# Kernel tuning notes

Measured on AMD Instinct MI355X. Metric: run time of the kernel, lower is better.

## Reference

```python
import jax, jax.numpy as jnp
import numpy as np
from jax import lax

N_KERNELS = 11
N_GRAMS = 3
EMB = 300
CONV_OUT = 128
B, QLEN, DLEN = 128, 30, 256


def _kernel_mus(n):
    mus = [1.0]
    bin_size = 2.0 / (n - 1)
    mus.append(1 - bin_size / 2)
    for i in range(1, n - 1):
        mus.append(mus[i] - bin_size)
    return mus


def _kernel_sigmas(n):
    bin_size = 2.0 / (n - 1)
    return [0.001] + [0.5 * bin_size] * (n - 1)


MU = jnp.asarray(np.array(_kernel_mus(N_KERNELS), dtype=np.float32))      # [K]
SIGMA = jnp.asarray(np.array(_kernel_sigmas(N_KERNELS), dtype=np.float32))  # [K]


def setup_inputs() -> dict:
    key = jax.random.key(0)
    ks = jax.random.split(key, 10)
    inp = {
        "query_embeddings": jax.random.normal(ks[0], (B, QLEN, EMB), jnp.float32),
        "document_embeddings": jax.random.normal(ks[1], (B, DLEN, EMB), jnp.float32),
        "query_pad_oov_mask": jnp.ones((B, QLEN), jnp.float32),
        "document_pad_oov_mask": jnp.ones((B, DLEN), jnp.float32),
    }
    # conv weights for n-gram sizes 1..3: [out_ch, in_ch, ksize]
    for i in range(1, N_GRAMS + 1):
        inp[f"conv_w{i}"] = jax.random.normal(ks[1 + i], (CONV_OUT, EMB, i), jnp.float32) * 0.05
        inp[f"conv_b{i}"] = jnp.zeros((CONV_OUT,), jnp.float32)
    inp["dense_w"] = jax.random.uniform(ks[9], (1, N_KERNELS * N_GRAMS * N_GRAMS), jnp.float32,
                                        minval=-0.014, maxval=0.014)
    return inp


def _conv_ngram(x, w, b):
    # x: [B, L, E]; w: [C, E, k]; right-pad by k-1 so output length == L (ConstantPad1d((0,k-1)))
    k = w.shape[-1]
    y = lax.conv_general_dilated(x.transpose(0, 2, 1), w, (1,), [(0, k - 1)],
                                 dimension_numbers=("NCH", "OIH", "NCH"))
    return jax.nn.relu(y + b[None, :, None]).transpose(0, 2, 1)  # [B, L, C]


def _kernel_pool(q, d, qd_mask, q_mask):
    # cosine matrix (AllenNLP CosineMatrixAttention: normalize with +1e-13 eps)
    qn = q / (jnp.linalg.norm(q, axis=-1, keepdims=True) + 1e-13)
    dn = d / (jnp.linalg.norm(d, axis=-1, keepdims=True) + 1e-13)
    cos = jnp.einsum("bqe,bde->bqd", qn, dn) * qd_mask  # [B, Q, D]
    # RBF soft-histogram kernels: [B, Q, D, K]
    k = jnp.exp(-(cos[..., None] - MU) ** 2 / (2.0 * SIGMA ** 2)) * qd_mask[..., None]
    per_kernel_query = k.sum(axis=2)  # [B, Q, K]
    log_pk = jnp.log(jnp.clip(per_kernel_query, 1e-10, None)) * 0.01
    return (log_pk * q_mask[..., None]).sum(axis=1)  # [B, K]


def reference(query_embeddings, document_embeddings, query_pad_oov_mask, document_pad_oov_mask,
              conv_w1, conv_b1, conv_w2, conv_b2, conv_w3, conv_b3, dense_w):
    qd_mask = query_pad_oov_mask[:, :, None] * document_pad_oov_mask[:, None, :]  # [B, Q, D]
    conv_params = [(conv_w1, conv_b1), (conv_w2, conv_b2), (conv_w3, conv_b3)]
    q_res = [_conv_ngram(query_embeddings, w, b) for w, b in conv_params]
    d_res = [_conv_ngram(document_embeddings, w, b) for w, b in conv_params]
    matched = [_kernel_pool(q_res[i], d_res[t], qd_mask, query_pad_oov_mask)
               for i in range(N_GRAMS) for t in range(N_GRAMS)]
    all_grams = jnp.concatenate(matched, axis=1)  # [B, K*9]
    return jnp.squeeze(all_grams @ dense_w.T, axis=1)  # [B]
```

## Files before the change

### kernel.cpp

```cpp
#include <hip/hip_runtime.h>
#include <math.h>


typedef __bf16 bf16x8 __attribute__((ext_vector_type(8)));
typedef float f32x4 __attribute__((ext_vector_type(4)));

#if __has_builtin(__builtin_amdgcn_exp2f)
#define EXP2F(x) __builtin_amdgcn_exp2f(x)
#else
#define EXP2F(x) exp2f(x)
#endif

#define AS_STRIDE 344

static __device__ __forceinline__ unsigned short f2bf(float f) {
  union { float f; unsigned int u; } v; v.f = f;
  unsigned int r = v.u + 0x7FFFu + ((v.u >> 16) & 1u);
  return (unsigned short)(r >> 16);
}

__global__ __launch_bounds__(256) void prep_w(
    const float* __restrict__ w1, const float* __restrict__ w2,
    const float* __restrict__ w3, unsigned short* __restrict__ wt2) {
  int idx = blockIdx.x * 256 + threadIdx.x;
  if (idx >= 245760) return;
  int jj   = idx & 7;
  int lane = (idx >> 3) & 63;
  int ec   = (idx >> 9) % 10;
  int cb   = (idx / 5120) & 7;
  int p    = idx / 40960;
  const float* w; int k, jt;
  if (p == 0)      { w = w1; k = 1; jt = 0; }
  else if (p <= 2) { w = w2; k = 2; jt = p - 1; }
  else             { w = w3; k = 3; jt = p - 3; }
  int c = cb * 16 + (lane & 15);
  int e = ec * 32 + (lane >> 4) * 8 + jj;
  float v = (e < 300) ? w[(c * 300 + e) * k + jt] : 0.0f;
  wt2[idx] = f2bf(v);
}

template<int NI>
__device__ __forceinline__ void conv_body(
    unsigned short* As, float* psq,
    const float* __restrict__ xs, int L, int l0, int b,
    const unsigned short* __restrict__ wt2,
    const float* __restrict__ b1, const float* __restrict__ b2,
    const float* __restrict__ b3,
    unsigned short* __restrict__ out) {
  constexpr int ROWS = NI * 16 + 2;
  constexpr int NR = NI * 16;
  const int t = threadIdx.x;
  const int w = __builtin_amdgcn_readfirstlane(t >> 6);
  const int lane = t & 63;
  const int quad = lane >> 4, lrow = lane & 15;

  for (int idx = t; idx < ROWS * 40; idx += 512) {
    int r = idx / 40, c = idx % 40;
    int l = l0 + r;
    int e = c * 8;
    float4 a = make_float4(0.f, 0.f, 0.f, 0.f);
    float4 cc = make_float4(0.f, 0.f, 0.f, 0.f);
    if (l < L) {
      const float* src = xs + (size_t)l * 300;
      if (e < 300)     a  = *reinterpret_cast<const float4*>(src + e);
      if (e + 4 < 300) cc = *reinterpret_cast<const float4*>(src + e + 4);
    }
    uint4 o;
    o.x = (unsigned int)f2bf(a.x) | ((unsigned int)f2bf(a.y) << 16);
    o.y = (unsigned int)f2bf(a.z) | ((unsigned int)f2bf(a.w) << 16);
    o.z = (unsigned int)f2bf(cc.x) | ((unsigned int)f2bf(cc.y) << 16);
    o.w = (unsigned int)f2bf(cc.z) | ((unsigned int)f2bf(cc.w) << 16);
    *reinterpret_cast<uint4*>(&As[r * AS_STRIDE + c * 8]) = o;
  }

  f32x4 acc[NI][3];
  #pragma unroll
  for (int ni = 0; ni < NI; ++ni)
    #pragma unroll
    for (int g = 0; g < 3; ++g) acc[ni][g] = (f32x4){0.f, 0.f, 0.f, 0.f};

  const unsigned short* wl = wt2 + (size_t)lane * 8;

  auto wfld = [&](bf16x8* dst, int ec) {
    #pragma unroll
    for (int p = 0; p < 6; ++p)
      dst[p] = *reinterpret_cast<const bf16x8*>(
          wl + ((((p * 8 + w) * 10 + ec) << 9)));
  };

  auto compute = [&](const bf16x8* wf, int ec) {
    bf16x8 xf[3][NI];
    #pragma unroll
    for (int j = 0; j < 3; ++j)
      #pragma unroll
      for (int ni = 0; ni < NI; ++ni)
        xf[j][ni] = *reinterpret_cast<const bf16x8*>(
            &As[(ni * 16 + lrow + j) * AS_STRIDE + ec * 32 + quad * 8]);
    const int PJ[6] = {0, 0, 1, 0, 1, 2};
    const int PG[6] = {0, 1, 1, 2, 2, 2};
    #pragma unroll
    for (int p = 0; p < 6; ++p)
      #pragma unroll
      for (int ni = 0; ni < NI; ++ni)
        acc[ni][PG[p]] = __builtin_amdgcn_mfma_f32_16x16x32_bf16(
            wf[p], xf[PJ[p]][ni], acc[ni][PG[p]], 0, 0, 0);
  };

  bf16x8 wfA[6], wfB[6];
  wfld(wfA, 0);
  __syncthreads();

  #pragma unroll
  for (int ec = 0; ec < 10; ec += 2) {
    wfld(wfB, ec + 1);
    compute(wfA, ec);
    if (ec + 2 < 10) wfld(wfA, ec + 2);
    compute(wfB, ec + 1);
  }

  const float* biases[3] = {b1, b2, b3};
  float4 bv[3];
  #pragma unroll
  for (int g = 0; g < 3; ++g)
    bv[g] = *reinterpret_cast<const float4*>(biases[g] + w * 16 + quad * 4);

  #pragma unroll
  for (int ni = 0; ni < NI; ++ni) {
    #pragma unroll
    for (int g = 0; g < 3; ++g) {
      float p = 0.f;
      #pragma unroll
      for (int r = 0; r < 4; ++r) {
        float y = fmaxf(acc[ni][g][r] + bv[g][r], 0.f);
        p += y * y;
      }
      p += __shfl_xor(p, 16);
      p += __shfl_xor(p, 32);
      if (lane < 16) psq[(w * 3 + g) * NR + ni * 16 + lrow] = p;
    }
  }
  __syncthreads();

  #pragma unroll
  for (int ni = 0; ni < NI; ++ni) {
    int row = ni * 16 + lrow;
    int l = l0 + row;
    if (l < L) {
      #pragma unroll
      for (int g = 0; g < 3; ++g) {
        float ssq = 0.f;
        #pragma unroll
        for (int wv = 0; wv < 8; ++wv) ssq += psq[(wv * 3 + g) * NR + row];
        float inv = 1.0f / (sqrtf(ssq) + 1e-13f);
        unsigned int pk[2];
        #pragma unroll
        for (int h = 0; h < 2; ++h) {
          float y0 = fmaxf(acc[ni][g][2 * h + 0] + bv[g][2 * h + 0], 0.f) * inv;
          float y1 = fmaxf(acc[ni][g][2 * h + 1] + bv[g][2 * h + 1], 0.f) * inv;
          pk[h] = (unsigned int)f2bf(y0) | ((unsigned int)f2bf(y1) << 16);
        }
        unsigned short* op = out + ((size_t)(g * 128 + b) * L + l) * 128 +
                             w * 16 + quad * 4;
        *reinterpret_cast<uint2*>(op) = make_uint2(pk[0], pk[1]);
      }
    }
  }
}

__global__ __launch_bounds__(512, 4) void conv_all(
    const float* __restrict__ qemb, const float* __restrict__ demb,
    const unsigned short* __restrict__ wt2,
    const float* __restrict__ b1, const float* __restrict__ b2,
    const float* __restrict__ b3,
    unsigned short* __restrict__ qn, unsigned short* __restrict__ dn) {
  __shared__ unsigned short As[34 * AS_STRIDE];
  __shared__ float psq[8 * 3 * 32];
  const int bi = blockIdx.x;
  if (bi < 1024)
    conv_body<2>(As, psq, demb + (size_t)(bi >> 3) * 256 * 300, 256,
                 (bi & 7) * 32, bi >> 3, wt2, b1, b2, b3, dn);
  else
    conv_body<2>(As, psq, qemb + (size_t)(bi - 1024) * 30 * 300, 30,
                 0, bi - 1024, wt2, b1, b2, b3, qn);
}

__global__ __launch_bounds__(512, 1) void pool_final(
    const unsigned short* __restrict__ qn, const unsigned short* __restrict__ dn,
    const float* __restrict__ qmask, const float* __restrict__ dmask,
    const float* __restrict__ dw, float* __restrict__ out) {
  const float A2[11] = {2.0f, 1.8f, 1.4f, 1.0f, 0.6f, 0.2f,
                        -0.2f, -0.6f, -1.0f, -1.4f, -1.8f};
  const float CC[11] = {-721347.52f, -58.429149f, -35.346028f, -18.033688f,
                        -6.4921277f, -0.72134752f, -0.72134752f, -6.4921277f,
                        -18.033688f, -35.346028f, -58.429149f};
  __shared__ float psum[2][3][4][330];
  __shared__ float wsum[8];
  const int t = threadIdx.x;
  const int wv   = t >> 6;
  const int slot = wv >> 2;
  const int sub  = wv & 3;
  const int lane = t & 63;
  const int quad = lane >> 4, l15 = lane & 15;
  const int u  = blockIdx.x * 2 + slot;
  const int tg = u >> 7;
  const int b  = u & 127;

  const unsigned short* dslab = dn + (size_t)(tg * 128 + b) * 256 * 128;
  float qmv[2];
  qmv[0] = qmask[b * 30 + l15];
  qmv[1] = (16 + l15 < 30) ? qmask[b * 30 + 16 + l15] : 0.0f;

  #pragma unroll 1
  for (int ig = 0; ig < 3; ++ig) {
    const unsigned short* qslab = qn + (size_t)(ig * 128 + b) * 30 * 128;
    bf16x8 bQ[2][4];
    #pragma unroll
    for (int ni = 0; ni < 2; ++ni)
      #pragma unroll
      for (int kt = 0; kt < 4; ++kt)
        bQ[ni][kt] = *reinterpret_cast<const bf16x8*>(
            qslab + (size_t)(ni * 16 + l15) * 128 + kt * 32 + quad * 8);

    float feat[2][11];
    #pragma unroll
    for (int ni = 0; ni < 2; ++ni)
      #pragma unroll
      for (int kk = 0; kk < 11; ++kk) feat[ni][kk] = 0.0f;

    #pragma unroll
    for (int half = 0; half < 2; ++half) {
      const int d0 = (sub * 2 + half) * 32;
      bf16x8 aD[2][4];
      #pragma unroll
      for (int mi = 0; mi < 2; ++mi)
        #pragma unroll
        for (int kt = 0; kt < 4; ++kt)
          aD[mi][kt] = *reinterpret_cast<const bf16x8*>(
              dslab + (size_t)(d0 + mi * 16 + l15) * 128 + kt * 32 + quad * 8);
      float dmv[2][4];
      #pragma unroll
      for (int mi = 0; mi < 2; ++mi)
        #pragma unroll
        for (int r = 0; r < 4; ++r)
          dmv[mi][r] = dmask[b * 256 + d0 + mi * 16 + quad * 4 + r];

      f32x4 acc[2][2];
      #pragma unroll
      for (int mi = 0; mi < 2; ++mi)
        #pragma unroll
        for (int ni = 0; ni < 2; ++ni) acc[mi][ni] = (f32x4){0.f, 0.f, 0.f, 0.f};
      #pragma unroll
      for (int kt = 0; kt < 4; ++kt)
        #pragma unroll
        for (int mi = 0; mi < 2; ++mi)
          #pragma unroll
          for (int ni = 0; ni < 2; ++ni)
            acc[mi][ni] = __builtin_amdgcn_mfma_f32_16x16x32_bf16(
                aD[mi][kt], bQ[ni][kt], acc[mi][ni], 0, 0, 0);

      #pragma unroll
      for (int mi = 0; mi < 2; ++mi) {
        #pragma unroll
        for (int r = 0; r < 4; ++r) {
          #pragma unroll
          for (int ni = 0; ni < 2; ++ni) {
            float m  = qmv[ni] * dmv[mi][r];
            float cm = acc[mi][ni][r] * m;
            float w0 = cm * -721347.52f;
            float w1c = cm * -72.134752f;
            #pragma unroll
            for (int kk = 0; kk < 11; ++kk) {
              float wk = (kk == 0) ? w0 : w1c;
              float e = EXP2F(fmaf(wk, cm - A2[kk], CC[kk]));
              feat[ni][kk] += e * m;
            }
          }
        }
      }
    }

    #pragma unroll
    for (int ni = 0; ni < 2; ++ni)
      #pragma unroll
      for (int kk = 0; kk < 11; ++kk) {
        float v = feat[ni][kk];
        v += __shfl_xor(v, 16);
        v += __shfl_xor(v, 32);
        feat[ni][kk] = v;
      }

    if (quad == 0) {
      #pragma unroll
      for (int ni = 0; ni < 2; ++ni) {
        int q = ni * 16 + l15;
        if (q < 30) {
          #pragma unroll
          for (int kk = 0; kk < 11; ++kk)
            psum[slot][ig][sub][q * 11 + kk] = feat[ni][kk];
        }
      }
    }
  }
  __syncthreads();

  float s = 0.0f;
  {
    const int tin = t & 255;
    for (int idx = tin; idx < 330; idx += 256) {
      int q = idx / 11, kk = idx % 11;
      float qm = qmask[b * 30 + q] * 0.01f;
      #pragma unroll
      for (int ig = 0; ig < 3; ++ig) {
        float v = psum[slot][ig][0][idx] + psum[slot][ig][1][idx]
                + psum[slot][ig][2][idx] + psum[slot][ig][3][idx];
        s += __logf(fmaxf(v, 1e-10f)) * qm * dw[(ig * 3 + tg) * 11 + kk];
      }
    }
    s += __shfl_xor(s, 1);  s += __shfl_xor(s, 2);  s += __shfl_xor(s, 4);
    s += __shfl_xor(s, 8);  s += __shfl_xor(s, 16); s += __shfl_xor(s, 32);
  }
  if (lane == 0) wsum[wv] = s;
  __syncthreads();
  if ((t & 255) == 0)
    atomicAdd(out + b, wsum[slot * 4 + 0] + wsum[slot * 4 + 1] +
                       wsum[slot * 4 + 2] + wsum[slot * 4 + 3]);
}

extern "C" void kernel_launch(void* const* d_in, const int* in_sizes, int n_in,
                              void* d_out, int out_size, void* d_ws, size_t ws_size,
                              hipStream_t stream) {
  const float* qemb  = (const float*)d_in[0];
  const float* demb  = (const float*)d_in[1];
  const float* qmask = (const float*)d_in[2];
  const float* dmask = (const float*)d_in[3];
  const float* w1 = (const float*)d_in[4];
  const float* b1 = (const float*)d_in[5];
  const float* w2 = (const float*)d_in[6];
  const float* b2 = (const float*)d_in[7];
  const float* w3 = (const float*)d_in[8];
  const float* b3 = (const float*)d_in[9];
  const float* dw = (const float*)d_in[10];

  unsigned short* ws  = (unsigned short*)d_ws;
  unsigned short* wt2 = ws;
  unsigned short* qn  = ws + 12042240;
  unsigned short* dn  = ws + 13516800;
  float* out = (float*)d_out;

  prep_w<<<960, 256, 0, stream>>>(w1, w2, w3, wt2);
  conv_all<<<1152, 512, 0, stream>>>(qemb, demb, wt2, b1, b2, b3, qn, dn);
  pool_final<<<192, 512, 0, stream>>>(qn, dn, qmask, dmask, dw, out);
}
```

Before: 183.5 us.

## Fuse conv and pooling into one persistent kernel with grid barrier

```diff
diff --git a/kernel.cpp b/kernel.cpp
--- a/kernel.cpp
+++ b/kernel.cpp
@@ -21,7 +21,9 @@
 
 __global__ __launch_bounds__(256) void prep_w(
     const float* __restrict__ w1, const float* __restrict__ w2,
-    const float* __restrict__ w3, unsigned short* __restrict__ wt2) {
+    const float* __restrict__ w3, unsigned short* __restrict__ wt2,
+    unsigned int* __restrict__ sync) {
+  if (blockIdx.x == 0 && threadIdx.x < 4) sync[threadIdx.x] = 0u;
   int idx = blockIdx.x * 256 + threadIdx.x;
   if (idx >= 245760) return;
   int jj   = idx & 7;
@@ -167,163 +169,178 @@
   }
 }
 
-__global__ __launch_bounds__(512, 4) void conv_all(
+struct ConvSm { unsigned short As[34 * AS_STRIDE]; float psq[8 * 3 * 32]; };
+union SmU {
+  ConvSm conv;
+  float psum[3][8][330];
+};
+
+__global__ __launch_bounds__(512, 4) void fused(
     const float* __restrict__ qemb, const float* __restrict__ demb,
+    const float* __restrict__ qmask, const float* __restrict__ dmask,
     const unsigned short* __restrict__ wt2,
     const float* __restrict__ b1, const float* __restrict__ b2,
     const float* __restrict__ b3,
-    unsigned short* __restrict__ qn, unsigned short* __restrict__ dn) {
-  __shared__ unsigned short As[34 * AS_STRIDE];
-  __shared__ float psq[8 * 3 * 32];
-  const int bi = blockIdx.x;
-  if (bi < 1024)
-    conv_body<2>(As, psq, demb + (size_t)(bi >> 3) * 256 * 300, 256,
-                 (bi & 7) * 32, bi >> 3, wt2, b1, b2, b3, dn);
-  else
-    conv_body<2>(As, psq, qemb + (size_t)(bi - 1024) * 30 * 300, 30,
-                 0, bi - 1024, wt2, b1, b2, b3, qn);
-}
-
-__global__ __launch_bounds__(512, 1) void pool_final(
-    const unsigned short* __restrict__ qn, const unsigned short* __restrict__ dn,
-    const float* __restrict__ qmask, const float* __restrict__ dmask,
-    const float* __restrict__ dw, float* __restrict__ out) {
-  const float A2[11] = {2.0f, 1.8f, 1.4f, 1.0f, 0.6f, 0.2f,
-                        -0.2f, -0.6f, -1.0f, -1.4f, -1.8f};
-  const float CC[11] = {-721347.52f, -58.429149f, -35.346028f, -18.033688f,
-                        -6.4921277f, -0.72134752f, -0.72134752f, -6.4921277f,
-                        -18.033688f, -35.346028f, -58.429149f};
-  __shared__ float psum[2][3][4][330];
+    const float* __restrict__ dw,
+    unsigned short* __restrict__ qn, unsigned short* __restrict__ dn,
+    unsigned int* __restrict__ sync, float* __restrict__ out) {
+  __shared__ SmU sm;
+  __shared__ int sbi;
   __shared__ float wsum[8];
   const int t = threadIdx.x;
-  const int wv   = t >> 6;
-  const int slot = wv >> 2;
-  const int sub  = wv & 3;
-  const int lane = t & 63;
-  const int quad = lane >> 4, l15 = lane & 15;
-  const int u  = blockIdx.x * 2 + slot;
-  const int tg = u >> 7;
-  const int b  = u & 127;
-
-  const unsigned short* dslab = dn + (size_t)(tg * 128 + b) * 256 * 128;
-  float qmv[2];
-  qmv[0] = qmask[b * 30 + l15];
-  qmv[1] = (16 + l15 < 30) ? qmask[b * 30 + 16 + l15] : 0.0f;
-
-  #pragma unroll 1
-  for (int ig = 0; ig < 3; ++ig) {
-    const unsigned short* qslab = qn + (size_t)(ig * 128 + b) * 30 * 128;
-    bf16x8 bQ[2][4];
-    #pragma unroll
-    for (int ni = 0; ni < 2; ++ni)
-      #pragma unroll
-      for (int kt = 0; kt < 4; ++kt)
-        bQ[ni][kt] = *reinterpret_cast<const bf16x8*>(
-            qslab + (size_t)(ni * 16 + l15) * 128 + kt * 32 + quad * 8);
-
-    float feat[2][11];
-    #pragma unroll
-    for (int ni = 0; ni < 2; ++ni)
-      #pragma unroll
-      for (int kk = 0; kk < 11; ++kk) feat[ni][kk] = 0.0f;
-
-    #pragma unroll
-    for (int half = 0; half < 2; ++half) {
-      const int d0 = (sub * 2 + half) * 32;
-      bf16x8 aD[2][4];
-      #pragma unroll
-      for (int mi = 0; mi < 2; ++mi)
-        #pragma unroll
-        for (int kt = 0; kt < 4; ++kt)
-          aD[mi][kt] = *reinterpret_cast<const bf16x8*>(
-              dslab + (size_t)(d0 + mi * 16 + l15) * 128 + kt * 32 + quad * 8);
-      float dmv[2][4];
-      #pragma unroll
-      for (int mi = 0; mi < 2; ++mi)
-        #pragma unroll
-        for (int r = 0; r < 4; ++r)
-          dmv[mi][r] = dmask[b * 256 + d0 + mi * 16 + quad * 4 + r];
-
-      f32x4 acc[2][2];
-      #pragma unroll
-      for (int mi = 0; mi < 2; ++mi)
-        #pragma unroll
-        for (int ni = 0; ni < 2; ++ni) acc[mi][ni] = (f32x4){0.f, 0.f, 0.f, 0.f};
-      #pragma unroll
-      for (int kt = 0; kt < 4; ++kt)
-        #pragma unroll
-        for (int mi = 0; mi < 2; ++mi)
-          #pragma unroll
-          for (int ni = 0; ni < 2; ++ni)
-            acc[mi][ni] = __builtin_amdgcn_mfma_f32_16x16x32_bf16(
-                aD[mi][kt], bQ[ni][kt], acc[mi][ni], 0, 0, 0);
-
-      #pragma unroll
-      for (int mi = 0; mi < 2; ++mi) {
-        #pragma unroll
-        for (int r = 0; r < 4; ++r) {
+
+  for (;;) {
+    __syncthreads();
+    if (t == 0) sbi = (int)atomicAdd(&sync[0], 1u);
+    __syncthreads();
+    const int bi = sbi;
+    if (bi >= 1152) break;
+    if (bi < 1024)
+      conv_body<2>(sm.conv.As, sm.conv.psq,
+                   demb + (size_t)(bi >> 3) * 256 * 300, 256,
+                   (bi & 7) * 32, bi >> 3, wt2, b1, b2, b3, dn);
+    else
+      conv_body<2>(sm.conv.As, sm.conv.psq,
+                   qemb + (size_t)(bi - 1024) * 30 * 300, 30,
+                   0, bi - 1024, wt2, b1, b2, b3, qn);
+  }
+
+  __syncthreads();
+  if (t == 0) {
+    __threadfence();
+    atomicAdd(&sync[1], 1u);
+    while (atomicAdd(&sync[1], 0u) < gridDim.x) __builtin_amdgcn_s_sleep(2);
+    __threadfence();
+  }
+  __syncthreads();
+
+  {
+    const float A2[11] = {2.0f, 1.8f, 1.4f, 1.0f, 0.6f, 0.2f,
+                          -0.2f, -0.6f, -1.0f, -1.4f, -1.8f};
+    const float CC[11] = {-721347.52f, -58.429149f, -35.346028f, -18.033688f,
+                          -6.4921277f, -0.72134752f, -0.72134752f, -6.4921277f,
+                          -18.033688f, -35.346028f, -58.429149f};
+    const int wv   = t >> 6;
+    const int lane = t & 63;
+    const int quad = lane >> 4, l15 = lane & 15;
+
+    for (;;) {
+      __syncthreads();
+      if (t == 0) sbi = (int)atomicAdd(&sync[2], 1u);
+      __syncthreads();
+      const int u = sbi;
+      if (u >= 384) break;
+      const int tg = u >> 7;
+      const int b  = u & 127;
+
+      const unsigned short* dslab = dn + (size_t)(tg * 128 + b) * 256 * 128;
+      float qmv[2];
+      qmv[0] = qmask[b * 30 + l15];
+      qmv[1] = (16 + l15 < 30) ? qmask[b * 30 + 16 + l15] : 0.0f;
+
+      #pragma unroll 1
+      for (int ig = 0; ig < 3; ++ig) {
+        const unsigned short* qslab = qn + (size_t)(ig * 128 + b) * 30 * 128;
+        bf16x8 bQ[2][4];
+        #pragma unroll
+        for (int ni = 0; ni < 2; ++ni)
+          #pragma unroll
+          for (int kt = 0; kt < 4; ++kt)
+            bQ[ni][kt] = *reinterpret_cast<const bf16x8*>(
+                qslab + (size_t)(ni * 16 + l15) * 128 + kt * 32 + quad * 8);
+
+        float feat[2][11];
+        #pragma unroll
+        for (int ni = 0; ni < 2; ++ni)
+          #pragma unroll
+          for (int kk = 0; kk < 11; ++kk) feat[ni][kk] = 0.0f;
+
+        #pragma unroll 1
+        for (int c = 0; c < 2; ++c) {
+          const int d0 = wv * 32 + c * 16;
+          bf16x8 aD[4];
+          #pragma unroll
+          for (int kt = 0; kt < 4; ++kt)
+            aD[kt] = *reinterpret_cast<const bf16x8*>(
+                dslab + (size_t)(d0 + l15) * 128 + kt * 32 + quad * 8);
+          float dmv[4];
+          #pragma unroll
+          for (int r = 0; r < 4; ++r)
+            dmv[r] = dmask[b * 256 + d0 + quad * 4 + r];
+
+          f32x4 acc[2];
+          acc[0] = (f32x4){0.f, 0.f, 0.f, 0.f};
+          acc[1] = (f32x4){0.f, 0.f, 0.f, 0.f};
+          #pragma unroll
+          for (int kt = 0; kt < 4; ++kt)
+            #pragma unroll
+            for (int ni = 0; ni < 2; ++ni)
+              acc[ni] = __builtin_amdgcn_mfma_f32_16x16x32_bf16(
+                  aD[kt], bQ[ni][kt], acc[ni], 0, 0, 0);
+
+          #pragma unroll
+          for (int r = 0; r < 4; ++r) {
+            #pragma unroll
+            for (int ni = 0; ni < 2; ++ni) {
+              float m  = qmv[ni] * dmv[r];
+              float cm = acc[ni][r] * m;
+              float w0 = cm * -721347.52f;
+              float w1c = cm * -72.134752f;
+              #pragma unroll
+              for (int kk = 0; kk < 11; ++kk) {
+                float wk = (kk == 0) ? w0 : w1c;
+                float e = EXP2F(fmaf(wk, cm - A2[kk], CC[kk]));
+                feat[ni][kk] += e * m;
+              }
+            }
+          }
+        }
+
+        #pragma unroll
+        for (int ni = 0; ni < 2; ++ni)
+          #pragma unroll
+          for (int kk = 0; kk < 11; ++kk) {
+            float v = feat[ni][kk];
+            v += __shfl_xor(v, 16);
+            v += __shfl_xor(v, 32);
+            feat[ni][kk] = v;
+          }
+
+        if (quad == 0) {
           #pragma unroll
           for (int ni = 0; ni < 2; ++ni) {
-            float m  = qmv[ni] * dmv[mi][r];
-            float cm = acc[mi][ni][r] * m;
-            float w0 = cm * -721347.52f;
-            float w1c = cm * -72.134752f;
-            #pragma unroll
-            for (int kk = 0; kk < 11; ++kk) {
-              float wk = (kk == 0) ? w0 : w1c;
-              float e = EXP2F(fmaf(wk, cm - A2[kk], CC[kk]));
-              feat[ni][kk] += e * m;
+            int q = ni * 16 + l15;
+            if (q < 30) {
+              #pragma unroll
+              for (int kk = 0; kk < 11; ++kk)
+                sm.psum[ig][wv][q * 11 + kk] = feat[ni][kk];
             }
           }
         }
       }
-    }
-
-    #pragma unroll
-    for (int ni = 0; ni < 2; ++ni)
-      #pragma unroll
-      for (int kk = 0; kk < 11; ++kk) {
-        float v = feat[ni][kk];
-        v += __shfl_xor(v, 16);
-        v += __shfl_xor(v, 32);
-        feat[ni][kk] = v;
-      }
-
-    if (quad == 0) {
-      #pragma unroll
-      for (int ni = 0; ni < 2; ++ni) {
-        int q = ni * 16 + l15;
-        if (q < 30) {
-          #pragma unroll
-          for (int kk = 0; kk < 11; ++kk)
-            psum[slot][ig][sub][q * 11 + kk] = feat[ni][kk];
+      __syncthreads();
+
+      float s = 0.0f;
+      if (t < 330) {
+        int q = t / 11, kk = t % 11;
+        float qm = qmask[b * 30 + q] * 0.01f;
+        #pragma unroll
+        for (int ig = 0; ig < 3; ++ig) {
+          float v = 0.f;
+          #pragma unroll
+          for (int sub = 0; sub < 8; ++sub) v += sm.psum[ig][sub][t];
+          s += __logf(fmaxf(v, 1e-10f)) * qm * dw[(ig * 3 + tg) * 11 + kk];
         }
       }
+      s += __shfl_xor(s, 1);  s += __shfl_xor(s, 2);  s += __shfl_xor(s, 4);
+      s += __shfl_xor(s, 8);  s += __shfl_xor(s, 16); s += __shfl_xor(s, 32);
+      if (lane == 0) wsum[wv] = s;
+      __syncthreads();
+      if (t == 0)
+        atomicAdd(out + b, wsum[0] + wsum[1] + wsum[2] + wsum[3] +
+                           wsum[4] + wsum[5] + wsum[6] + wsum[7]);
     }
   }
-  __syncthreads();
-
-  float s = 0.0f;
-  {
-    const int tin = t & 255;
-    for (int idx = tin; idx < 330; idx += 256) {
-      int q = idx / 11, kk = idx % 11;
-      float qm = qmask[b * 30 + q] * 0.01f;
-      #pragma unroll
-      for (int ig = 0; ig < 3; ++ig) {
-        float v = psum[slot][ig][0][idx] + psum[slot][ig][1][idx]
-                + psum[slot][ig][2][idx] + psum[slot][ig][3][idx];
-        s += __logf(fmaxf(v, 1e-10f)) * qm * dw[(ig * 3 + tg) * 11 + kk];
-      }
-    }
-    s += __shfl_xor(s, 1);  s += __shfl_xor(s, 2);  s += __shfl_xor(s, 4);
-    s += __shfl_xor(s, 8);  s += __shfl_xor(s, 16); s += __shfl_xor(s, 32);
-  }
-  if (lane == 0) wsum[wv] = s;
-  __syncthreads();
-  if ((t & 255) == 0)
-    atomicAdd(out + b, wsum[slot * 4 + 0] + wsum[slot * 4 + 1] +
-                       wsum[slot * 4 + 2] + wsum[slot * 4 + 3]);
 }
 
 extern "C" void kernel_launch(void* const* d_in, const int* in_sizes, int n_in,
@@ -343,11 +360,12 @@
 
   unsigned short* ws  = (unsigned short*)d_ws;
   unsigned short* wt2 = ws;
+  unsigned int*   syncp = (unsigned int*)(ws + 245760);
   unsigned short* qn  = ws + 12042240;
   unsigned short* dn  = ws + 13516800;
   float* out = (float*)d_out;
 
-  prep_w<<<960, 256, 0, stream>>>(w1, w2, w3, wt2);
-  conv_all<<<1152, 512, 0, stream>>>(qemb, demb, wt2, b1, b2, b3, qn, dn);
-  pool_final<<<192, 512, 0, stream>>>(qn, dn, qmask, dmask, dw, out);
-}
+  prep_w<<<960, 256, 0, stream>>>(w1, w2, w3, wt2, syncp);
+  fused<<<512, 512, 0, stream>>>(qemb, demb, qmask, dmask, wt2,
+                                 b1, b2, b3, dw, qn, dn, syncp, out);
+}
```

Measured after the change: 274.0 us. 49.3% more time.
